# Optimization experiments

Hardware: AMD Instinct MI355X
Metric: run time of the kernel (lower is better)

## Reference

```python
import jax, jax.numpy as jnp
import numpy as np

B, H, N, D = 2, 12, 2048, 64
M = int(D * np.log(D))          # 266 performer random features
E3 = 3 * D                      # performer value hidden size = head_dim*3
DH2 = 2 * D                     # predictor enc hidden = head_dim*2
T = 128                         # attention_predictor_length
CHUNK = 128                     # chunk size for causal linear attention scan
KERNEL_EPS = 1e-3               # performer generalized-kernel epsilon
D_EPS = 1e-6                    # denominator epsilon (added to k_cumsum)
LN_EPS = 1e-5


def setup_inputs() -> dict:
    key = jax.random.key(0)
    ks = jax.random.split(key, 10)
    return {
        "q": jax.random.normal(ks[0], (B, H, N, D), jnp.float32),
        "k": jax.random.normal(ks[1], (B, H, N, D), jnp.float32),
        "v3": jax.random.normal(ks[2], (B, H, N, E3), jnp.float32),
        "proj": jax.random.normal(ks[3], (M, D), jnp.float32),
        "enc_w": jax.random.normal(ks[4], (E3, DH2), jnp.float32) * 0.05,
        "enc_b": jnp.zeros((DH2,), jnp.float32),
        "ln_g": jnp.ones((DH2,), jnp.float32),
        "ln_b": jnp.zeros((DH2,), jnp.float32),
        "dec_w": jax.random.normal(ks[5], (DH2, T), jnp.float32) * 0.05,
        "dec_b": jnp.zeros((T,), jnp.float32),
    }


def _generalized_features(x, proj):
    # performer generalized attention kernel: relu((x / d^0.25) @ proj^T) + eps
    dn = 1.0 / (x.shape[-1] ** 0.25)
    xp = jnp.einsum("bhnd,md->bhnm", x * dn, proj)
    return jax.nn.relu(xp) + KERNEL_EPS


def _causal_linear_attention(qf, kf, v):
    # qf, kf: [B,H,N,M]; v: [B,H,N,E]. Chunked recurrent form of
    # out[n] = (qf[n] . cumsum(kf)[n])^-1 * qf[n] @ cumsum(kf[m] v[m]^T)[n]
    nE = v.shape[-1]
    nc = N // CHUNK
    qc = qf.reshape(B, H, nc, CHUNK, M).transpose(2, 0, 1, 3, 4)
    kc = kf.reshape(B, H, nc, CHUNK, M).transpose(2, 0, 1, 3, 4)
    vc = v.reshape(B, H, nc, CHUNK, nE).transpose(2, 0, 1, 3, 4)
    mask = jnp.tril(jnp.ones((CHUNK, CHUNK), qf.dtype))

    def step(carry, inp):
        ksum, S = carry                      # [B,H,M], [B,H,M,E]
        q_c, k_c, v_c = inp                  # [B,H,C,M], [B,H,C,M], [B,H,C,E]
        qk = jnp.einsum("bhim,bhjm->bhij", q_c, k_c) * mask  # causal within chunk
        # denominator: qf[n] . (k_cumsum[n] + eps)
        d = (jnp.einsum("bhcm,bhm->bhc", q_c, ksum)
             + qk.sum(-1)
             + D_EPS * q_c.sum(-1))
        out = (jnp.einsum("bhcm,bhme->bhce", q_c, S)
               + jnp.einsum("bhij,bhje->bhie", qk, v_c)) / d[..., None]
        ksum = ksum + k_c.sum(axis=2)
        S = S + jnp.einsum("bhcm,bhce->bhme", k_c, v_c)
        return (ksum, S), out

    init = (jnp.zeros((B, H, M), qf.dtype), jnp.zeros((B, H, M, nE), qf.dtype))
    _, outs = jax.lax.scan(step, init, (qc, kc, vc))
    return outs.transpose(1, 2, 0, 3, 4).reshape(B, H, N, nE)


def reference(q, k, v3, proj, enc_w, enc_b, ln_g, ln_b, dec_w, dec_b):
    qf = _generalized_features(q, proj)
    kf = _generalized_features(k, proj)
    ctx = _causal_linear_attention(qf, kf, v3)            # [B,H,N,3D]
    # attention predictor: Linear -> LayerNorm -> GELU -> Linear -> softmax
    h = jnp.einsum("bhne,ec->bhnc", ctx, enc_w) + enc_b    # [B,H,N,2D]
    mu = h.mean(-1, keepdims=True)
    var = ((h - mu) ** 2).mean(-1, keepdims=True)
    h = (h - mu) * jax.lax.rsqrt(var + LN_EPS) * ln_g + ln_b
    h = jax.nn.gelu(h, approximate=False)
    scores = jnp.einsum("bhnc,ct->bhnt", h, dec_w) + dec_b  # [B,H,N,T]
    est_probs = jax.nn.softmax(scores, axis=-1)
    return ctx, est_probs
```

## Files before the change

### kernel.cpp

```cpp
#include <hip/hip_runtime.h>
#include <hip/hip_bf16.h>
#include <math.h>

constexpr int Bn = 2, Hn = 12, BHn = 24;
constexpr int Nn = 2048, Dn = 64;
constexpr int Mn = 266, MPn = 272;
constexpr int E3n = 192, DHn = 128, Tn = 128;
constexpr int Cn = 128, NCn = 16;

#define DNRM 0.35355339059327373f
#define KEPS 1e-3f
#define DEPS 1e-6f
#define LNEPS 1e-5f

static const size_t OFF_QF   = 0;
static const size_t OFF_KF   = 26738688;
static const size_t OFF_QK   = 53477376;
static const size_t OFF_D    = 66060288;
static const size_t OFF_KPRE = 66256896;
static const size_t OFF_S    = 66674688;
static const size_t OFF_WT   = OFF_KF;
static const size_t WS_NEED  = 106782720;

using bf16x8 = __attribute__((ext_vector_type(8))) short;
using f32x4  = __attribute__((ext_vector_type(4))) float;

__device__ inline float u2f(unsigned int u) {
  union { float f; unsigned int i; } c; c.i = u << 16; return c.f;
}
__device__ inline unsigned short f2u(float x) {
  __hip_bfloat16 h = __float2bfloat16(x);
  unsigned short u; __builtin_memcpy(&u, &h, 2); return u;
}
__device__ inline void unpack8(uint4 v, float* a) {
  a[0] = u2f(v.x & 0xffffu); a[1] = u2f(v.x >> 16);
  a[2] = u2f(v.y & 0xffffu); a[3] = u2f(v.y >> 16);
  a[4] = u2f(v.z & 0xffffu); a[5] = u2f(v.z >> 16);
  a[6] = u2f(v.w & 0xffffu); a[7] = u2f(v.w >> 16);
}
__device__ inline ushort4 f4tobf(float4 v) {
  ushort4 o;
  o.x = f2u(v.x); o.y = f2u(v.y); o.z = f2u(v.z); o.w = f2u(v.w);
  return o;
}

__global__ __launch_bounds__(256) void k_features_mfma(
    const float* __restrict__ q, const float* __restrict__ k,
    const float* __restrict__ proj,
    unsigned short* __restrict__ qf, unsigned short* __restrict__ kf) {
  __shared__ unsigned short at[64][40];
  __shared__ unsigned short bt[272][40];
  const float* x = (blockIdx.y == 0) ? q : k;
  unsigned short* outp = (blockIdx.y == 0) ? qf : kf;
  int tid = threadIdx.x;
  int w = tid >> 6, l = tid & 63;
  int l16 = l & 15, lg = l >> 4;
  int r0 = blockIdx.x * 64;

  f32x4 acc[17] = {};
  for (int kt = 0; kt < 2; ++kt) {
    int k0 = kt * 32;
    __syncthreads();
    #pragma unroll
    for (int p = 0; p < 2; ++p) {
      int idx = tid + p * 256;
      int row = idx >> 3, kq = idx & 7;
      float4 v = *(const float4*)(x + (size_t)(r0 + row) * Dn + k0 + kq * 4);
      *(ushort4*)&at[row][kq * 4] = f4tobf(v);
    }
    for (int idx = tid; idx < 2176; idx += 256) {
      int mq = idx >> 3, kq = idx & 7;
      float4 v = make_float4(0.f, 0.f, 0.f, 0.f);
      if (mq < Mn) v = *(const float4*)(proj + (size_t)mq * Dn + k0 + kq * 4);
      *(ushort4*)&bt[mq][kq * 4] = f4tobf(v);
    }
    __syncthreads();
    bf16x8 a = *(const bf16x8*)((const char*)&at[0][0] + (w*16 + l16) * 80 + lg * 16);
    #pragma unroll
    for (int ct = 0; ct < 17; ++ct) {
      bf16x8 b = *(const bf16x8*)((const char*)&bt[0][0] + (ct*16 + l16) * 80 + lg * 16);
      acc[ct] = __builtin_amdgcn_mfma_f32_16x16x32_bf16(a, b, acc[ct], 0, 0, 0);
    }
  }
  #pragma unroll
  for (int ct = 0; ct < 17; ++ct)
    #pragma unroll
    for (int reg = 0; reg < 4; ++reg) {
      int row = r0 + w*16 + lg*4 + reg;
      int m = ct*16 + l16;
      float val = 0.f;
      if (m < Mn) val = fmaxf(acc[ct][reg] * DNRM, 0.f) + KEPS;
      outp[(size_t)row * MPn + m] = f2u(val);
    }
}

__global__ __launch_bounds__(256) void k_kprefix(float* __restrict__ kpre) {
  int bh = blockIdx.x; int tid = threadIdx.x;
  for (int m = tid; m < MPn; m += 256) {
    float v[NCn];
    #pragma unroll
    for (int c = 0; c < NCn; ++c) v[c] = kpre[((size_t)bh * NCn + c) * MPn + m];
    float acc = 0.f;
    #pragma unroll
    for (int c = 0; c < NCn; ++c) {
      kpre[((size_t)bh * NCn + c) * MPn + m] = acc;
      acc += v[c];
    }
  }
}

__global__ __launch_bounds__(256) void k_qk_mfma(
    const unsigned short* __restrict__ qf,
    const unsigned short* __restrict__ kf,
    const float* __restrict__ kpre,
    unsigned short* __restrict__ qkout,
    float* __restrict__ dden) {
  __shared__ unsigned short at[128][40];
  __shared__ unsigned short ktl[128][40];
  __shared__ float kp[MPn];
  __shared__ float rs_lds[128];
  int blk = blockIdx.x;
  int bh = blk >> 4, c = blk & 15;
  int tid = threadIdx.x;
  int w = tid >> 6, l = tid & 63;
  int l16 = l & 15, lg = l >> 4;
  size_t qbase = ((size_t)bh * Nn + (size_t)c * Cn) * MPn;
  size_t rbase = (size_t)bh * Nn + (size_t)c * Cn;
  for (int m = tid; m < MPn; m += 256) kp[m] = kpre[((size_t)bh * NCn + c) * MPn + m];

  f32x4 acc[2][8] = {};
  for (int kt = 0; kt < 9; ++kt) {
    int mt = kt * 32;
    __syncthreads();
    #pragma unroll
    for (int p = 0; p < 2; ++p) {
      int idx = tid * 8 + p * 2048;
      int r = idx >> 5, kk = idx & 31;
      uint4 va = make_uint4(0u,0u,0u,0u), vk = make_uint4(0u,0u,0u,0u);
      if (mt + kk < MPn) {
        va = *(const uint4*)(qf + qbase + (size_t)r * MPn + mt + kk);
        vk = *(const uint4*)(kf + qbase + (size_t)r * MPn + mt + kk);
      }
      *(uint4*)((char*)&at[0][0] + r * 80 + kk * 2) = va;
      *(uint4*)((char*)&ktl[0][0] + r * 80 + kk * 2) = vk;
    }
    __syncthreads();
    bf16x8 a0 = *(const bf16x8*)((const char*)&at[0][0] + (w*32 + l16) * 80 + lg * 16);
    bf16x8 a1 = *(const bf16x8*)((const char*)&at[0][0] + (w*32 + 16 + l16) * 80 + lg * 16);
    #pragma unroll
    for (int ct = 0; ct < 8; ++ct) {
      bf16x8 b = *(const bf16x8*)((const char*)&ktl[0][0] + (ct*16 + l16) * 80 + lg * 16);
      acc[0][ct] = __builtin_amdgcn_mfma_f32_16x16x32_bf16(a0, b, acc[0][ct], 0, 0, 0);
      acc[1][ct] = __builtin_amdgcn_mfma_f32_16x16x32_bf16(a1, b, acc[1][ct], 0, 0, 0);
    }
  }
  size_t qkbase = (size_t)blk * (Cn * Cn);
  float rs[2][4] = {};
  #pragma unroll
  for (int rt = 0; rt < 2; ++rt)
    #pragma unroll
    for (int ct = 0; ct < 8; ++ct)
      #pragma unroll
      for (int reg = 0; reg < 4; ++reg) {
        int row = w*32 + rt*16 + lg*4 + reg;
        int col = ct*16 + l16;
        float v = (col <= row) ? acc[rt][ct][reg] : 0.f;
        qkout[qkbase + (size_t)row * Cn + col] = f2u(v);
        rs[rt][reg] += v;
      }
  #pragma unroll
  for (int rt = 0; rt < 2; ++rt)
    #pragma unroll
    for (int reg = 0; reg < 4; ++reg) {
      float s = rs[rt][reg];
      s += __shfl_xor(s, 1); s += __shfl_xor(s, 2);
      s += __shfl_xor(s, 4); s += __shfl_xor(s, 8);
      rs[rt][reg] = s;
    }
  if (l16 == 0) {
    #pragma unroll
    for (int rt = 0; rt < 2; ++rt)
      #pragma unroll
      for (int reg = 0; reg < 4; ++reg)
        rs_lds[w*32 + rt*16 + lg*4 + reg] = rs[rt][reg];
  }
  __syncthreads();
  if (tid < 128) {
    float dot = 0.f, qs = 0.f;
    const unsigned short* qrow = qf + qbase + (size_t)tid * MPn;
    for (int m = 0; m < MPn; m += 8) {
      uint4 v = *(const uint4*)(qrow + m);
      float a[8]; unpack8(v, a);
      #pragma unroll
      for (int t = 0; t < 8; ++t) { dot += a[t] * kp[m + t]; qs += a[t]; }
    }
    dden[rbase + tid] = rs_lds[tid] + dot + DEPS * qs;
  }
}

__global__ __launch_bounds__(256) void k_schunk_mfma(
    const unsigned short* __restrict__ kf,
    const float* __restrict__ v3,
    unsigned short* __restrict__ ST,
    float* __restrict__ kpre) {
  __shared__ unsigned short at[64][40];
  __shared__ unsigned short bt[272][36];
  int blk = blockIdx.x, ey = blockIdx.y;
  int bh = blk >> 4, c = blk & 15;
  int e0 = ey * 64;
  int tid = threadIdx.x;
  int w = tid >> 6, l = tid & 63;
  int l16 = l & 15, lg = l >> 4;
  size_t vbase = ((size_t)bh * Nn + (size_t)c * Cn) * E3n + e0;
  size_t kbase = ((size_t)bh * Nn + (size_t)c * Cn) * MPn;

  f32x4 acc[17] = {};
  float ks0 = 0.f, ks1 = 0.f;
  for (int kt = 0; kt < 4; ++kt) {
    int jt = kt * 32;
    __syncthreads();
    #pragma unroll
    for (int p = 0; p < 2; ++p) {
      int idx = tid + p * 256;
      int j = idx & 31, eq = idx >> 5;
      float4 v = *(const float4*)(v3 + vbase + (size_t)(jt + j) * E3n + eq * 4);
      at[eq*4+0][j] = f2u(v.x); at[eq*4+1][j] = f2u(v.y);
      at[eq*4+2][j] = f2u(v.z); at[eq*4+3][j] = f2u(v.w);
    }
    for (int idx = tid; idx < 1088; idx += 256) {
      int j = idx & 31, mq = idx >> 5;
      uint4 v = *(const uint4*)(kf + kbase + (size_t)(jt + j) * MPn + mq * 8);
      unsigned short tmp[8]; __builtin_memcpy(tmp, &v, 16);
      #pragma unroll
      for (int t = 0; t < 8; ++t) bt[mq*8+t][j] = tmp[t];
    }
    __syncthreads();
    bf16x8 a = *(const bf16x8*)((const char*)&at[0][0] + (w*16 + l16) * 80 + lg * 16);
    #pragma unroll
    for (int ct = 0; ct < 17; ++ct) {
      bf16x8 b = *(const bf16x8*)((const char*)&bt[0][0] + (ct*16 + l16) * 72 + lg * 16);
      acc[ct] = __builtin_amdgcn_mfma_f32_16x16x32_bf16(a, b, acc[ct], 0, 0, 0);
    }
    if (ey == 0) {
      #pragma unroll
      for (int jq = 0; jq < 4; ++jq) {
        uint4 v = *(const uint4*)((const char*)&bt[0][0] + tid * 72 + jq * 16);
        float a8[8]; unpack8(v, a8);
        #pragma unroll
        for (int t = 0; t < 8; ++t) ks0 += a8[t];
      }
      if (tid < 16) {
        #pragma unroll
        for (int jq = 0; jq < 4; ++jq) {
          uint4 v = *(const uint4*)((const char*)&bt[0][0] + (tid + 256) * 72 + jq * 16);
          float a8[8]; unpack8(v, a8);
          #pragma unroll
          for (int t = 0; t < 8; ++t) ks1 += a8[t];
        }
      }
    }
  }
  size_t stbase = (size_t)blk * MPn * E3n + (size_t)e0 * MPn;
  #pragma unroll
  for (int ct = 0; ct < 17; ++ct)
    #pragma unroll
    for (int reg = 0; reg < 4; ++reg) {
      int e_loc = w*16 + lg*4 + reg;
      ST[stbase + (size_t)e_loc * MPn + ct*16 + l16] = f2u(acc[ct][reg]);
    }
  if (ey == 0) {
    kpre[((size_t)bh * NCn + c) * MPn + tid] = ks0;
    if (tid < 16)
      kpre[((size_t)bh * NCn + c) * MPn + tid + 256] = ks1;
  }
}

__global__ __launch_bounds__(256) void k_wt(const float* __restrict__ enc_w,
    const float* __restrict__ dec_w, unsigned short* __restrict__ ewt,
    unsigned short* __restrict__ dwt) {
  int i = blockIdx.x * 256 + threadIdx.x;
  if (i < 128 * 192) {
    int n = i / 192, e = i - n * 192;
    ewt[i] = f2u(enc_w[(size_t)e * DHn + n]);
  } else {
    int j = i - 128 * 192;
    int t = j >> 7, c = j & 127;
    dwt[(size_t)t * DHn + c] = f2u(dec_w[(size_t)c * Tn + t]);
  }
}

__global__ __launch_bounds__(256) void k_sprefix(unsigned short* __restrict__ S) {
  int bh = blockIdx.x / 51, sub = blockIdx.x % 51;
  int idx4 = sub * 256 + threadIdx.x;
  size_t off = (size_t)idx4 * 4;
  ushort4 v[NCn];
  #pragma unroll
  for (int c = 0; c < NCn; ++c)
    v[c] = *(const ushort4*)(S + ((size_t)(bh * NCn + c)) * MPn * E3n + off);
  float a0 = 0.f, a1 = 0.f, a2 = 0.f, a3 = 0.f;
  #pragma unroll
  for (int c = 0; c < NCn; ++c) {
    ushort4 o;
    unsigned short* op = (unsigned short*)&o;
    op[0] = f2u(a0); op[1] = f2u(a1); op[2] = f2u(a2); op[3] = f2u(a3);
    *(ushort4*)(S + ((size_t)(bh * NCn + c)) * MPn * E3n + off) = o;
    a0 += u2f(v[c].x); a1 += u2f(v[c].y); a2 += u2f(v[c].z); a3 += u2f(v[c].w);
  }
}

__global__ __launch_bounds__(256) void k_ctx_mfma(
    const unsigned short* __restrict__ qf,
    const unsigned short* __restrict__ qkm,
    const unsigned short* __restrict__ ST,
    const float* __restrict__ v3,
    const float* __restrict__ dden,
    float* __restrict__ ctx) {
  __shared__ unsigned short at[128][40];
  __shared__ unsigned short bt[64][40];
  __shared__ float dd[128];
  int blk = blockIdx.x, ey = blockIdx.y;
  int bh = blk >> 4, c = blk & 15;
  int e0 = ey * 64;
  int tid = threadIdx.x;
  int w = tid >> 6, l = tid & 63;
  int l16 = l & 15, lg = l >> 4;
  size_t qbase = ((size_t)bh * Nn + (size_t)c * Cn) * MPn;
  size_t sbase = (size_t)blk * MPn * E3n + (size_t)e0 * MPn;
  size_t rbase = (size_t)bh * Nn + (size_t)c * Cn;
  if (tid < 128) dd[tid] = dden[rbase + tid];

  f32x4 acc[2][4] = {};
  for (int kt = 0; kt < 9; ++kt) {
    int mt = kt * 32;
    __syncthreads();
    #pragma unroll
    for (int p = 0; p < 2; ++p) {
      int idx = tid * 8 + p * 2048;
      int r = idx >> 5, kk = idx & 31;
      uint4 v = make_uint4(0u,0u,0u,0u);
      if (mt + kk < MPn) v = *(const uint4*)(qf + qbase + (size_t)r * MPn + mt + kk);
      *(uint4*)((char*)&at[0][0] + r * 80 + kk * 2) = v;
    }
    {
      int r = tid >> 2, kk = (tid & 3) * 8;
      uint4 v = make_uint4(0u,0u,0u,0u);
      if (mt + kk < MPn) v = *(const uint4*)(ST + sbase + (size_t)r * MPn + mt + kk);
      *(uint4*)((char*)&bt[0][0] + r * 80 + kk * 2) = v;
    }
    __syncthreads();
    bf16x8 a0 = *(const bf16x8*)((const char*)&at[0][0] + (w*32 + l16) * 80 + lg * 16);
    bf16x8 a1 = *(const bf16x8*)((const char*)&at[0][0] + (w*32 + 16 + l16) * 80 + lg * 16);
    #pragma unroll
    for (int ct = 0; ct < 4; ++ct) {
      bf16x8 b = *(const bf16x8*)((const char*)&bt[0][0] + (ct*16 + l16) * 80 + lg * 16);
      acc[0][ct] = __builtin_amdgcn_mfma_f32_16x16x32_bf16(a0, b, acc[0][ct], 0, 0, 0);
      acc[1][ct] = __builtin_amdgcn_mfma_f32_16x16x32_bf16(a1, b, acc[1][ct], 0, 0, 0);
    }
  }
  size_t kkbase = (size_t)blk * (Cn * Cn);
  size_t vb3 = ((size_t)bh * Nn + (size_t)c * Cn) * E3n + e0;
  for (int kt = 0; kt < 4; ++kt) {
    int jt = kt * 32;
    __syncthreads();
    #pragma unroll
    for (int p = 0; p < 2; ++p) {
      int idx = tid * 8 + p * 2048;
      int r = idx >> 5, kk = idx & 31;
      uint4 v = *(const uint4*)(qkm + kkbase + (size_t)r * Cn + jt + kk);
      *(uint4*)((char*)&at[0][0] + r * 80 + kk * 2) = v;
    }
    #pragma unroll
    for (int p = 0; p < 2; ++p) {
      int idx = tid + p * 256;
      int j = idx & 31, eq = idx >> 5;
      float4 v = *(const float4*)(v3 + vb3 + (size_t)(jt + j) * E3n + eq * 4);
      bt[eq*4+0][j] = f2u(v.x); bt[eq*4+1][j] = f2u(v.y);
      bt[eq*4+2][j] = f2u(v.z); bt[eq*4+3][j] = f2u(v.w);
    }
    __syncthreads();
    bf16x8 a0 = *(const bf16x8*)((const char*)&at[0][0] + (w*32 + l16) * 80 + lg * 16);
    bf16x8 a1 = *(const bf16x8*)((const char*)&at[0][0] + (w*32 + 16 + l16) * 80 + lg * 16);
    #pragma unroll
    for (int ct = 0; ct < 4; ++ct) {
      bf16x8 b = *(const bf16x8*)((const char*)&bt[0][0] + (ct*16 + l16) * 80 + lg * 16);
      acc[0][ct] = __builtin_amdgcn_mfma_f32_16x16x32_bf16(a0, b, acc[0][ct], 0, 0, 0);
      acc[1][ct] = __builtin_amdgcn_mfma_f32_16x16x32_bf16(a1, b, acc[1][ct], 0, 0, 0);
    }
  }
  #pragma unroll
  for (int rt = 0; rt < 2; ++rt)
    #pragma unroll
    for (int ct = 0; ct < 4; ++ct)
      #pragma unroll
      for (int reg = 0; reg < 4; ++reg) {
        int row = w*32 + rt*16 + lg*4 + reg;
        float inv = 1.f / dd[row];
        ctx[(rbase + row) * (size_t)E3n + e0 + ct*16 + l16] = acc[rt][ct][reg] * inv;
      }
}

__global__ __launch_bounds__(256) void k_pred_fused(
    const float* __restrict__ ctx,
    const unsigned short* __restrict__ ewt,
    const unsigned short* __restrict__ dwt,
    const float* __restrict__ enc_b, const float* __restrict__ ln_g,
    const float* __restrict__ ln_b, const float* __restrict__ dec_b,
    float* __restrict__ probs) {
  __shared__ unsigned short at[128][40];
  __shared__ unsigned short bt[128][40];
  __shared__ unsigned short ht[128][200];
  int tid = threadIdx.x;
  int w = tid >> 6, l = tid & 63;
  int l16 = l & 15, lg = l >> 4;
  size_t r0 = (size_t)blockIdx.x * 128;

  float ebv[8], ggv[8], llv[8], dbv[8];
  #pragma unroll
  for (int ct = 0; ct < 8; ++ct) {
    ebv[ct] = enc_b[ct*16 + l16];
    ggv[ct] = ln_g[ct*16 + l16];
    llv[ct] = ln_b[ct*16 + l16];
    dbv[ct] = dec_b[ct*16 + l16];
  }

  f32x4 acc1[2][8] = {};
  for (int kt = 0; kt < 6; ++kt) {
    int k0 = kt * 32;
    __syncthreads();
    #pragma unroll
    for (int p = 0; p < 4; ++p) {
      int idx = tid + p * 256;
      int row = idx >> 3, kq = idx & 7;
      float4 v = *(const float4*)(ctx + (r0 + row) * E3n + k0 + kq * 4);
      *(ushort4*)&at[row][kq * 4] = f4tobf(v);
    }
    #pragma unroll
    for (int p = 0; p < 2; ++p) {
      int idx = tid + p * 256;
      int n = idx >> 2, kq = idx & 3;
      *(uint4*)&bt[n][kq * 8] = *(const uint4*)(ewt + (size_t)n * E3n + k0 + kq * 8);
    }
    __syncthreads();
    bf16x8 a0 = *(const bf16x8*)((const char*)&at[0][0] + (w*32 + l16) * 80 + lg * 16);
    bf16x8 a1 = *(const bf16x8*)((const char*)&at[0][0] + (w*32 + 16 + l16) * 80 + lg * 16);
    #pragma unroll
    for (int ct = 0; ct < 8; ++ct) {
      bf16x8 b = *(const bf16x8*)((const char*)&bt[0][0] + (ct*16 + l16) * 80 + lg * 16);
      acc1[0][ct] = __builtin_amdgcn_mfma_f32_16x16x32_bf16(a0, b, acc1[0][ct], 0, 0, 0);
      acc1[1][ct] = __builtin_amdgcn_mfma_f32_16x16x32_bf16(a1, b, acc1[1][ct], 0, 0, 0);
    }
  }
  #pragma unroll
  for (int rt = 0; rt < 2; ++rt) {
    #pragma unroll
    for (int reg = 0; reg < 4; ++reg) {
      float hv[8];
      float s = 0.f, s2 = 0.f;
      #pragma unroll
      for (int ct = 0; ct < 8; ++ct) {
        float v = acc1[rt][ct][reg] + ebv[ct];
        hv[ct] = v; s += v; s2 += v * v;
      }
      #pragma unroll
      for (int m = 1; m < 16; m <<= 1) { s += __shfl_xor(s, m); s2 += __shfl_xor(s2, m); }
      float mu = s * (1.f / 128.f);
      float var = s2 * (1.f / 128.f) - mu * mu;
      float rsq = rsqrtf(var + LNEPS);
      int row = w*32 + rt*16 + lg*4 + reg;
      #pragma unroll
      for (int ct = 0; ct < 8; ++ct) {
        float v = (hv[ct] - mu) * rsq * ggv[ct] + llv[ct];
        v = 0.5f * v * (1.f + erff(v * 0.70710678118654752f));
        ht[row][ct*16 + l16] = f2u(v);
      }
    }
  }
  f32x4 acc2[2][8] = {};
  for (int kt = 0; kt < 4; ++kt) {
    int c0 = kt * 32;
    __syncthreads();
    #pragma unroll
    for (int p = 0; p < 2; ++p) {
      int idx = tid + p * 256;
      int t = idx >> 2, kq = idx & 3;
      *(uint4*)&bt[t][kq * 8] = *(const uint4*)(dwt + (size_t)t * DHn + c0 + kq * 8);
    }
    __syncthreads();
    bf16x8 a0 = *(const bf16x8*)&ht[w*32 + l16][c0 + lg*8];
    bf16x8 a1 = *(const bf16x8*)&ht[w*32 + 16 + l16][c0 + lg*8];
    #pragma unroll
    for (int ct = 0; ct < 8; ++ct) {
      bf16x8 b = *(const bf16x8*)((const char*)&bt[0][0] + (ct*16 + l16) * 80 + lg * 16);
      acc2[0][ct] = __builtin_amdgcn_mfma_f32_16x16x32_bf16(a0, b, acc2[0][ct], 0, 0, 0);
      acc2[1][ct] = __builtin_amdgcn_mfma_f32_16x16x32_bf16(a1, b, acc2[1][ct], 0, 0, 0);
    }
  }
  #pragma unroll
  for (int rt = 0; rt < 2; ++rt) {
    #pragma unroll
    for (int reg = 0; reg < 4; ++reg) {
      float sv[8];
      float m = -1e30f;
      #pragma unroll
      for (int ct = 0; ct < 8; ++ct) {
        sv[ct] = acc2[rt][ct][reg] + dbv[ct];
        m = fmaxf(m, sv[ct]);
      }
      #pragma unroll
      for (int mm = 1; mm < 16; mm <<= 1) m = fmaxf(m, __shfl_xor(m, mm));
      float s = 0.f;
      #pragma unroll
      for (int ct = 0; ct < 8; ++ct) { sv[ct] = expf(sv[ct] - m); s += sv[ct]; }
      #pragma unroll
      for (int mm = 1; mm < 16; mm <<= 1) s += __shfl_xor(s, mm);
      float inv = 1.f / s;
      int row = w*32 + rt*16 + lg*4 + reg;
      #pragma unroll
      for (int ct = 0; ct < 8; ++ct)
        probs[(r0 + row) * (size_t)Tn + ct*16 + l16] = sv[ct] * inv;
    }
  }
}

extern "C" void kernel_launch(void* const* d_in, const int* in_sizes, int n_in,
                              void* d_out, int out_size, void* d_ws, size_t ws_size,
                              hipStream_t stream) {
  const float* q     = (const float*)d_in[0];
  const float* k     = (const float*)d_in[1];
  const float* v3    = (const float*)d_in[2];
  const float* proj  = (const float*)d_in[3];
  const float* enc_w = (const float*)d_in[4];
  const float* enc_b = (const float*)d_in[5];
  const float* ln_g  = (const float*)d_in[6];
  const float* ln_b  = (const float*)d_in[7];
  const float* dec_w = (const float*)d_in[8];
  const float* dec_b = (const float*)d_in[9];
  float* out = (float*)d_out;
  char* ws = (char*)d_ws;
  if (ws_size < WS_NEED) return;

  unsigned short* qf   = (unsigned short*)(ws + OFF_QF);
  unsigned short* kf   = (unsigned short*)(ws + OFF_KF);
  unsigned short* qk   = (unsigned short*)(ws + OFF_QK);
  float*          dden = (float*)(ws + OFF_D);
  float*          kpre = (float*)(ws + OFF_KPRE);
  unsigned short* ST   = (unsigned short*)(ws + OFF_S);
  unsigned short* ewt  = (unsigned short*)(ws + OFF_WT);
  unsigned short* dwt  = (unsigned short*)(ws + OFF_WT + 49152);
  float* ctx   = out;
  float* probs = out + (size_t)BHn * Nn * E3n;

  k_features_mfma<<<dim3(BHn * Nn / 64, 2), 256, 0, stream>>>(q, k, proj, qf, kf);
  k_schunk_mfma <<<dim3(BHn * NCn, 3),  256, 0, stream>>>(kf, v3, ST, kpre);
  k_kprefix     <<<dim3(BHn),           256, 0, stream>>>(kpre);
  k_qk_mfma     <<<dim3(BHn * NCn),     256, 0, stream>>>(qf, kf, kpre, qk, dden);
  k_wt          <<<dim3(160),           256, 0, stream>>>(enc_w, dec_w, ewt, dwt);
  k_sprefix     <<<dim3(BHn * 51),      256, 0, stream>>>(ST);
  k_ctx_mfma    <<<dim3(BHn * NCn, 3),  256, 0, stream>>>(qf, qk, ST, v3, dden, ctx);
  k_pred_fused  <<<dim3(BHn * Nn / 128),256, 0, stream>>>(ctx, ewt, dwt, enc_b, ln_g,
                                                          ln_b, dec_b, probs);
}
```

Measured before the change: 169.5 us.

## Merge the three E-slice blocks into one 768-thread block in schunk and ctx

Both the chunk-state kernel and the context kernel now launch a single 768-thread block per chunk that covers all 192 value columns, instead of three 256-thread blocks each covering 64. Within the block, 12 waves are split into row and column groups. The kf tile (schunk) and the qf/qk tiles (ctx) are then staged once per chunk instead of three times, cutting redundant global loads and LDS fills. The cost is fewer blocks (384), larger LDS per block and bigger blocks, which may lower occupancy and scheduling flexibility.

```diff
diff --git a/kernel.cpp b/kernel.cpp
--- a/kernel.cpp
+++ b/kernel.cpp
@@ -198,36 +198,35 @@
   }
 }
 
-__global__ __launch_bounds__(256) void k_schunk_mfma(
+__global__ __launch_bounds__(768) void k_schunk_mfma(
     const unsigned short* __restrict__ kf,
     const float* __restrict__ v3,
     unsigned short* __restrict__ ST,
     float* __restrict__ kpre) {
-  __shared__ unsigned short at[64][40];
+  __shared__ unsigned short at[192][40];
   __shared__ unsigned short bt[272][36];
-  int blk = blockIdx.x, ey = blockIdx.y;
+  int blk = blockIdx.x;
   int bh = blk >> 4, c = blk & 15;
-  int e0 = ey * 64;
   int tid = threadIdx.x;
   int w = tid >> 6, l = tid & 63;
   int l16 = l & 15, lg = l >> 4;
-  size_t vbase = ((size_t)bh * Nn + (size_t)c * Cn) * E3n + e0;
+  size_t vbase = ((size_t)bh * Nn + (size_t)c * Cn) * E3n;
   size_t kbase = ((size_t)bh * Nn + (size_t)c * Cn) * MPn;
 
   f32x4 acc[17] = {};
-  float ks0 = 0.f, ks1 = 0.f;
+  float ks = 0.f;
   for (int kt = 0; kt < 4; ++kt) {
     int jt = kt * 32;
     __syncthreads();
     #pragma unroll
     for (int p = 0; p < 2; ++p) {
-      int idx = tid + p * 256;
+      int idx = tid + p * 768;
       int j = idx & 31, eq = idx >> 5;
       float4 v = *(const float4*)(v3 + vbase + (size_t)(jt + j) * E3n + eq * 4);
       at[eq*4+0][j] = f2u(v.x); at[eq*4+1][j] = f2u(v.y);
       at[eq*4+2][j] = f2u(v.z); at[eq*4+3][j] = f2u(v.w);
     }
-    for (int idx = tid; idx < 1088; idx += 256) {
+    for (int idx = tid; idx < 1088; idx += 768) {
       int j = idx & 31, mq = idx >> 5;
       uint4 v = *(const uint4*)(kf + kbase + (size_t)(jt + j) * MPn + mq * 8);
       unsigned short tmp[8]; __builtin_memcpy(tmp, &v, 16);
@@ -241,26 +240,17 @@
       bf16x8 b = *(const bf16x8*)((const char*)&bt[0][0] + (ct*16 + l16) * 72 + lg * 16);
       acc[ct] = __builtin_amdgcn_mfma_f32_16x16x32_bf16(a, b, acc[ct], 0, 0, 0);
     }
-    if (ey == 0) {
+    if (tid < MPn) {
       #pragma unroll
       for (int jq = 0; jq < 4; ++jq) {
         uint4 v = *(const uint4*)((const char*)&bt[0][0] + tid * 72 + jq * 16);
         float a8[8]; unpack8(v, a8);
         #pragma unroll
-        for (int t = 0; t < 8; ++t) ks0 += a8[t];
-      }
-      if (tid < 16) {
-        #pragma unroll
-        for (int jq = 0; jq < 4; ++jq) {
-          uint4 v = *(const uint4*)((const char*)&bt[0][0] + (tid + 256) * 72 + jq * 16);
-          float a8[8]; unpack8(v, a8);
-          #pragma unroll
-          for (int t = 0; t < 8; ++t) ks1 += a8[t];
-        }
-      }
-    }
-  }
-  size_t stbase = (size_t)blk * MPn * E3n + (size_t)e0 * MPn;
+        for (int t = 0; t < 8; ++t) ks += a8[t];
+      }
+    }
+  }
+  size_t stbase = (size_t)blk * MPn * E3n;
   #pragma unroll
   for (int ct = 0; ct < 17; ++ct)
     #pragma unroll
@@ -268,11 +258,8 @@
       int e_loc = w*16 + lg*4 + reg;
       ST[stbase + (size_t)e_loc * MPn + ct*16 + l16] = f2u(acc[ct][reg]);
     }
-  if (ey == 0) {
-    kpre[((size_t)bh * NCn + c) * MPn + tid] = ks0;
-    if (tid < 16)
-      kpre[((size_t)bh * NCn + c) * MPn + tid + 256] = ks1;
-  }
+  if (tid < MPn)
+    kpre[((size_t)bh * NCn + c) * MPn + tid] = ks;
 }
 
 __global__ __launch_bounds__(256) void k_wt(const float* __restrict__ enc_w,
@@ -308,7 +295,7 @@
   }
 }
 
-__global__ __launch_bounds__(256) void k_ctx_mfma(
+__global__ __launch_bounds__(768) void k_ctx_mfma(
     const unsigned short* __restrict__ qf,
     const unsigned short* __restrict__ qkm,
     const unsigned short* __restrict__ ST,
@@ -316,16 +303,16 @@
     const float* __restrict__ dden,
     float* __restrict__ ctx) {
   __shared__ unsigned short at[128][40];
-  __shared__ unsigned short bt[64][40];
+  __shared__ unsigned short bt[192][40];
   __shared__ float dd[128];
-  int blk = blockIdx.x, ey = blockIdx.y;
+  int blk = blockIdx.x;
   int bh = blk >> 4, c = blk & 15;
-  int e0 = ey * 64;
   int tid = threadIdx.x;
   int w = tid >> 6, l = tid & 63;
   int l16 = l & 15, lg = l >> 4;
+  int wr = w & 3, we = w >> 2;
   size_t qbase = ((size_t)bh * Nn + (size_t)c * Cn) * MPn;
-  size_t sbase = (size_t)blk * MPn * E3n + (size_t)e0 * MPn;
+  size_t sbase = (size_t)blk * MPn * E3n;
   size_t rbase = (size_t)bh * Nn + (size_t)c * Cn;
   if (tid < 128) dd[tid] = dden[rbase + tid];
 
@@ -333,10 +320,8 @@
   for (int kt = 0; kt < 9; ++kt) {
     int mt = kt * 32;
     __syncthreads();
-    #pragma unroll
-    for (int p = 0; p < 2; ++p) {
-      int idx = tid * 8 + p * 2048;
-      int r = idx >> 5, kk = idx & 31;
+    if (tid < 512) {
+      int r = tid >> 2, kk = (tid & 3) * 8;
       uint4 v = make_uint4(0u,0u,0u,0u);
       if (mt + kk < MPn) v = *(const uint4*)(qf + qbase + (size_t)r * MPn + mt + kk);
       *(uint4*)((char*)&at[0][0] + r * 80 + kk * 2) = v;
@@ -348,41 +333,39 @@
       *(uint4*)((char*)&bt[0][0] + r * 80 + kk * 2) = v;
     }
     __syncthreads();
-    bf16x8 a0 = *(const bf16x8*)((const char*)&at[0][0] + (w*32 + l16) * 80 + lg * 16);
-    bf16x8 a1 = *(const bf16x8*)((const char*)&at[0][0] + (w*32 + 16 + l16) * 80 + lg * 16);
+    bf16x8 a0 = *(const bf16x8*)((const char*)&at[0][0] + (wr*32 + l16) * 80 + lg * 16);
+    bf16x8 a1 = *(const bf16x8*)((const char*)&at[0][0] + (wr*32 + 16 + l16) * 80 + lg * 16);
     #pragma unroll
     for (int ct = 0; ct < 4; ++ct) {
-      bf16x8 b = *(const bf16x8*)((const char*)&bt[0][0] + (ct*16 + l16) * 80 + lg * 16);
+      bf16x8 b = *(const bf16x8*)((const char*)&bt[0][0] + (we*64 + ct*16 + l16) * 80 + lg * 16);
       acc[0][ct] = __builtin_amdgcn_mfma_f32_16x16x32_bf16(a0, b, acc[0][ct], 0, 0, 0);
       acc[1][ct] = __builtin_amdgcn_mfma_f32_16x16x32_bf16(a1, b, acc[1][ct], 0, 0, 0);
     }
   }
   size_t kkbase = (size_t)blk * (Cn * Cn);
-  size_t vb3 = ((size_t)bh * Nn + (size_t)c * Cn) * E3n + e0;
+  size_t vb3 = ((size_t)bh * Nn + (size_t)c * Cn) * E3n;
   for (int kt = 0; kt < 4; ++kt) {
     int jt = kt * 32;
     __syncthreads();
-    #pragma unroll
-    for (int p = 0; p < 2; ++p) {
-      int idx = tid * 8 + p * 2048;
-      int r = idx >> 5, kk = idx & 31;
+    if (tid < 512) {
+      int r = tid >> 2, kk = (tid & 3) * 8;
       uint4 v = *(const uint4*)(qkm + kkbase + (size_t)r * Cn + jt + kk);
       *(uint4*)((char*)&at[0][0] + r * 80 + kk * 2) = v;
     }
     #pragma unroll
     for (int p = 0; p < 2; ++p) {
-      int idx = tid + p * 256;
+      int idx = tid + p * 768;
       int j = idx & 31, eq = idx >> 5;
       float4 v = *(const float4*)(v3 + vb3 + (size_t)(jt + j) * E3n + eq * 4);
       bt[eq*4+0][j] = f2u(v.x); bt[eq*4+1][j] = f2u(v.y);
       bt[eq*4+2][j] = f2u(v.z); bt[eq*4+3][j] = f2u(v.w);
     }
     __syncthreads();
-    bf16x8 a0 = *(const bf16x8*)((const char*)&at[0][0] + (w*32 + l16) * 80 + lg * 16);
-    bf16x8 a1 = *(const bf16x8*)((const char*)&at[0][0] + (w*32 + 16 + l16) * 80 + lg * 16);
+    bf16x8 a0 = *(const bf16x8*)((const char*)&at[0][0] + (wr*32 + l16) * 80 + lg * 16);
+    bf16x8 a1 = *(const bf16x8*)((const char*)&at[0][0] + (wr*32 + 16 + l16) * 80 + lg * 16);
     #pragma unroll
     for (int ct = 0; ct < 4; ++ct) {
-      bf16x8 b = *(const bf16x8*)((const char*)&bt[0][0] + (ct*16 + l16) * 80 + lg * 16);
+      bf16x8 b = *(const bf16x8*)((const char*)&bt[0][0] + (we*64 + ct*16 + l16) * 80 + lg * 16);
       acc[0][ct] = __builtin_amdgcn_mfma_f32_16x16x32_bf16(a0, b, acc[0][ct], 0, 0, 0);
       acc[1][ct] = __builtin_amdgcn_mfma_f32_16x16x32_bf16(a1, b, acc[1][ct], 0, 0, 0);
     }
@@ -393,9 +376,9 @@
     for (int ct = 0; ct < 4; ++ct)
       #pragma unroll
       for (int reg = 0; reg < 4; ++reg) {
-        int row = w*32 + rt*16 + lg*4 + reg;
+        int row = wr*32 + rt*16 + lg*4 + reg;
         float inv = 1.f / dd[row];
-        ctx[(rbase + row) * (size_t)E3n + e0 + ct*16 + l16] = acc[rt][ct][reg] * inv;
+        ctx[(rbase + row) * (size_t)E3n + we*64 + ct*16 + l16] = acc[rt][ct][reg] * inv;
       }
 }
 
@@ -551,12 +534,12 @@
   float* probs = out + (size_t)BHn * Nn * E3n;
 
   k_features_mfma<<<dim3(BHn * Nn / 64, 2), 256, 0, stream>>>(q, k, proj, qf, kf);
-  k_schunk_mfma <<<dim3(BHn * NCn, 3),  256, 0, stream>>>(kf, v3, ST, kpre);
+  k_schunk_mfma <<<dim3(BHn * NCn),     768, 0, stream>>>(kf, v3, ST, kpre);
   k_kprefix     <<<dim3(BHn),           256, 0, stream>>>(kpre);
   k_qk_mfma     <<<dim3(BHn * NCn),     256, 0, stream>>>(qf, kf, kpre, qk, dden);
   k_wt          <<<dim3(160),           256, 0, stream>>>(enc_w, dec_w, ewt, dwt);
   k_sprefix     <<<dim3(BHn * 51),      256, 0, stream>>>(ST);
-  k_ctx_mfma    <<<dim3(BHn * NCn, 3),  256, 0, stream>>>(qf, qk, ST, v3, dden, ctx);
+  k_ctx_mfma    <<<dim3(BHn * NCn),     768, 0, stream>>>(qf, qk, ST, v3, dden, ctx);
   k_pred_fused  <<<dim3(BHn * Nn / 128),256, 0, stream>>>(ctx, ewt, dwt, enc_b, ln_g,
                                                           ln_b, dec_b, probs);
 }
```

Result: faster. 156.9 us (-7.4%).
